# Performance work log

Measured on AMD Instinct MI355X. Metric: run time of the kernel, lower is better.

Reference implementation:

```python
import jax, jax.numpy as jnp
import numpy as np
from jax import lax

B, T, E, H = 16, 1024, 512, 1024


def setup_inputs() -> dict:
    key = jax.random.key(0)
    ks = jax.random.split(key, 10)
    s = 0.1
    return {
        "x":   jax.random.normal(ks[0], (B, T, E), jnp.float32),
        # reset gate: sigmoid(x@Wxr + h@Whr + br)
        "Wxr": jax.random.normal(ks[1], (E, H), jnp.float32) * s,
        "Whr": jax.random.normal(ks[2], (H, H), jnp.float32) * s,
        "br":  jax.random.normal(ks[3], (H,), jnp.float32) * s,
        # update gate: sigmoid(x@Wxz + h@Whz + bz)
        "Wxz": jax.random.normal(ks[4], (E, H), jnp.float32) * s,
        "Whz": jax.random.normal(ks[5], (H, H), jnp.float32) * s,
        "bz":  jax.random.normal(ks[6], (H,), jnp.float32) * s,
        # candidate: tanh(r * (h@Wh) + x@Wi + b)
        "Wi":  jax.random.normal(ks[7], (E, H), jnp.float32) * s,
        "Wh":  jax.random.normal(ks[8], (H, H), jnp.float32) * s,
        "b":   jax.random.normal(ks[9], (H,), jnp.float32) * s,
    }


def reference(x, Wxr, Whr, br, Wxz, Whz, bz, Wi, Wh, b):
    # Batch all input-to-hidden projections across time up front.
    xr = jnp.einsum("bte,eh->bth", x, Wxr) + br  # [B,T,H]
    xz = jnp.einsum("bte,eh->bth", x, Wxz) + bz
    xi = jnp.einsum("bte,eh->bth", x, Wi) + b

    def step(h, inp):
        xr_t, xz_t, xi_t = inp  # each [B,H]
        r = jax.nn.sigmoid(xr_t + h @ Whr)
        z = jax.nn.sigmoid(xz_t + h @ Whz)
        cand = jnp.tanh(r * (h @ Wh) + xi_t)
        h_new = z * h + (1.0 - z) * cand
        return h_new, h_new

    h0 = jnp.zeros((x.shape[0], Wh.shape[0]), x.dtype)
    # scan over time: move T to leading axis
    _, hs = lax.scan(step, h0, (xr.transpose(1, 0, 2), xz.transpose(1, 0, 2), xi.transpose(1, 0, 2)))
    return hs.transpose(1, 0, 2)  # [B,T,H]
```

## Files before the change

kernel.cpp:

```cpp
#include <hip/hip_runtime.h>
#include <hip/hip_bf16.h>
#include <cstddef>
#include <cstdint>

static constexpr int BB = 16;
static constexpr int TT = 1024;
static constexpr int EE = 512;
static constexpr int HH = 1024;

static constexpr int NG   = 4;
static constexpr int GBLK = 64;
static constexpr int BPG  = 4;
static constexpr int COLS = 16;

using u32 = unsigned int;
using u64 = unsigned long long;
typedef float f32x4 __attribute__((ext_vector_type(4)));

__device__ __forceinline__ float st_load(const float* p) { return *p; }
__device__ __forceinline__ float st_load(const __hip_bfloat16* p) { return __bfloat162float(*p); }
__device__ __forceinline__ void st_store(float* p, float v) { *p = v; }
__device__ __forceinline__ void st_store(__hip_bfloat16* p, float v) { *p = __float2bfloat16(v); }

__device__ __forceinline__ void llc_load(f32x4& d, const f32x4* p) {
    asm volatile("global_load_dwordx4 %0, %1, off sc0 sc1" : "=v"(d) : "v"(p));
}
__device__ __forceinline__ void llc_drain() {
    asm volatile("s_waitcnt vmcnt(0)" ::: "memory");
    __builtin_amdgcn_sched_barrier(0);
}

#define FMA4(ACC, S, W)                         \
    (ACC).x = fmaf((S), (W).x, (ACC).x);        \
    (ACC).y = fmaf((S), (W).y, (ACC).y);        \
    (ACC).z = fmaf((S), (W).z, (ACC).z);        \
    (ACC).w = fmaf((S), (W).w, (ACC).w);

template <typename ST>
__global__ __launch_bounds__(256) void proj_kernel(
    const float* __restrict__ x,
    const float* __restrict__ Wxr, const float* __restrict__ br,
    const float* __restrict__ Wxz, const float* __restrict__ bz,
    const float* __restrict__ Wi,  const float* __restrict__ bi,
    ST* __restrict__ xr_out, ST* __restrict__ xz_out, float* __restrict__ xi_out,
    u32* __restrict__ bar)
{
    __shared__ float xT[16][68];
    __shared__ float wB[3][16][64];

    const int tid = threadIdx.x;
    if (blockIdx.x == 0 && blockIdx.y == 0) bar[tid] = 0u;

    const int tx = tid & 15, ty = tid >> 4;
    const int m0 = blockIdx.y * 64, n0 = blockIdx.x * 64;
    const float* Wg[3] = {Wxr, Wxz, Wi};

    float4 acc[3][4];
#pragma unroll
    for (int g = 0; g < 3; ++g)
#pragma unroll
        for (int i = 0; i < 4; ++i) acc[g][i] = make_float4(0.f, 0.f, 0.f, 0.f);

    const int xrow = tid >> 2, xk = (tid & 3) * 4;
    const int wk = tid >> 4, wn = (tid & 15) * 4;

    for (int k0 = 0; k0 < EE; k0 += 16) {
        float4 xv = *(const float4*)(x + (size_t)(m0 + xrow) * EE + k0 + xk);
        xT[xk + 0][xrow] = xv.x;
        xT[xk + 1][xrow] = xv.y;
        xT[xk + 2][xrow] = xv.z;
        xT[xk + 3][xrow] = xv.w;
#pragma unroll
        for (int g = 0; g < 3; ++g) {
            float4 wv = *(const float4*)(Wg[g] + (size_t)(k0 + wk) * HH + n0 + wn);
            *(float4*)&wB[g][wk][wn] = wv;
        }
        __syncthreads();
#pragma unroll
        for (int kk = 0; kk < 16; ++kk) {
            float4 a  = *(const float4*)&xT[kk][ty * 4];
            float4 w0 = *(const float4*)&wB[0][kk][tx * 4];
            float4 w1 = *(const float4*)&wB[1][kk][tx * 4];
            float4 w2 = *(const float4*)&wB[2][kk][tx * 4];
            float as[4] = {a.x, a.y, a.z, a.w};
#pragma unroll
            for (int i = 0; i < 4; ++i) {
                FMA4(acc[0][i], as[i], w0);
                FMA4(acc[1][i], as[i], w1);
                FMA4(acc[2][i], as[i], w2);
            }
        }
        __syncthreads();
    }

    float4 bv0 = *(const float4*)(br + n0 + tx * 4);
    float4 bv1 = *(const float4*)(bz + n0 + tx * 4);
    float4 bv2 = *(const float4*)(bi + n0 + tx * 4);
#pragma unroll
    for (int i = 0; i < 4; ++i) {
        size_t m = (size_t)m0 + ty * 4 + i;
        size_t off = m * HH + n0 + tx * 4;
        float4 v0 = acc[0][i]; v0.x += bv0.x; v0.y += bv0.y; v0.z += bv0.z; v0.w += bv0.w;
        float4 v1 = acc[1][i]; v1.x += bv1.x; v1.y += bv1.y; v1.z += bv1.z; v1.w += bv1.w;
        float4 v2 = acc[2][i]; v2.x += bv2.x; v2.y += bv2.y; v2.z += bv2.z; v2.w += bv2.w;
        st_store(xr_out + off + 0, v0.x); st_store(xr_out + off + 1, v0.y);
        st_store(xr_out + off + 2, v0.z); st_store(xr_out + off + 3, v0.w);
        st_store(xz_out + off + 0, v1.x); st_store(xz_out + off + 1, v1.y);
        st_store(xz_out + off + 2, v1.z); st_store(xz_out + off + 3, v1.w);
        *(float4*)(xi_out + off) = v2;
    }
}

__device__ __forceinline__ float row16_allreduce(float v) {
    int y;
    y = __builtin_amdgcn_update_dpp(0, __float_as_int(v), 0xB1, 0xF, 0xF, true);
    v += __int_as_float(y);
    y = __builtin_amdgcn_update_dpp(0, __float_as_int(v), 0x4E, 0xF, 0xF, true);
    v += __int_as_float(y);
    y = __builtin_amdgcn_update_dpp(0, __float_as_int(v), 0x124, 0xF, 0xF, true);
    v += __int_as_float(y);
    y = __builtin_amdgcn_update_dpp(0, __float_as_int(v), 0x128, 0xF, 0xF, true);
    v += __int_as_float(y);
    return v;
}

__device__ __forceinline__ void xbar(u32* ctr, unsigned target) {
    __syncthreads();
    if (threadIdx.x == 0) {
        asm volatile("s_waitcnt vmcnt(0)" ::: "memory");
        __builtin_amdgcn_sched_barrier(0);
        __hip_atomic_fetch_add(ctr, 1u, __ATOMIC_RELAXED, __HIP_MEMORY_SCOPE_AGENT);
        while (__hip_atomic_load(ctr, __ATOMIC_RELAXED, __HIP_MEMORY_SCOPE_AGENT) < target) {
            __builtin_amdgcn_s_sleep(1);
        }
        __builtin_amdgcn_sched_barrier(0);
    }
    __syncthreads();
}

template <typename ST>
__global__ __launch_bounds__(512, 1) void scan_kernel(
    const ST* __restrict__ xr, const ST* __restrict__ xz,
    const float* __restrict__ Whr, const float* __restrict__ Whz, const float* __restrict__ Wh,
    float* __restrict__ out,
    float* __restrict__ hbuf,
    u32* __restrict__ bar)
{
    __shared__ f32x4 hs[BPG * 256];
    __shared__ float red[8][4][48];
    __shared__ float pre[48][4];

    const int tid = threadIdx.x, bid = blockIdx.x;
    const int lane = tid & 63, wv = tid >> 6;
    const int cgg = lane >> 4, kslo = lane & 15;
    const int ks = wv * 16 + kslo;
    const int group = bid >> 6, gb = bid & 63;
    const int n0 = gb * COLS;
    u32* ctr = bar + group * 64;

    float wreg[12][8];
    {
        const float* WG[3] = {Whr, Whz, Wh};
#pragma unroll
        for (int u = 0; u < 12; ++u) {
            int ugc = cgg * 12 + u;
            const float* W = WG[ugc >> 4];
            int col = n0 + (ugc & 15);
#pragma unroll
            for (int j = 0; j < 8; ++j)
                wreg[u][j] = W[(size_t)(ks * 8 + j) * HH + col];
        }
    }

    if (tid < 64)
        __hip_atomic_store(&hbuf[bid * 64 + tid], 0.f, __ATOMIC_RELAXED, __HIP_MEMORY_SCOPE_AGENT);

    float pxr = 0.f, pxz = 0.f, pxi = 0.f;
    const int tb4 = tid >> 4, tc = tid & 15;
    const int tbg = group * BPG + tb4;
    if (tid < 64) {
        size_t idx = (size_t)(tbg * TT + 0) * HH + n0 + tc;
        pxr = st_load(xr + idx); pxz = st_load(xz + idx); pxi = out[idx];
    }

    unsigned bstep = 1;
    xbar(ctr, bstep * GBLK); ++bstep;

    for (int t = 0; t < TT; ++t) {
        const f32x4* hin = (const f32x4*)(hbuf + (size_t)(t & 1) * (BB * HH) + group * BPG * HH);
        float* hout = hbuf + (size_t)((t + 1) & 1) * (BB * HH) + group * BPG * HH;

        f32x4 tmp0, tmp1;
        int q0 = (tid + (gb << 3)) & 1023;
        int q1 = (tid + 512 + (gb << 3)) & 1023;
        llc_load(tmp0, hin + q0);
        llc_load(tmp1, hin + q1);
        llc_drain();
        {
            int s0 = q0 & 255, s1 = q1 & 255;
            hs[(q0 & 0x300) | (s0 ^ ((s0 >> 3) & 7))] = tmp0;
            hs[(q1 & 0x300) | (s1 ^ ((s1 >> 3) & 7))] = tmp1;
        }
        __syncthreads();

        float pacc[4][12];
#pragma unroll
        for (int b = 0; b < 4; ++b)
#pragma unroll
            for (int u = 0; u < 12; ++u) pacc[b][u] = 0.f;

        const int s0 = 2 * ks;
        const int c0 = (s0 >> 3) & 7;
        const int sl0 = s0 ^ c0;
#pragma unroll
        for (int b = 0; b < 4; ++b) {
            f32x4 ha = hs[(b << 8) | sl0];
            f32x4 hb = hs[(b << 8) | (sl0 ^ 1)];
#pragma unroll
            for (int u = 0; u < 12; ++u) {
                float a = pacc[b][u];
                a = fmaf(ha[0], wreg[u][0], a);
                a = fmaf(ha[1], wreg[u][1], a);
                a = fmaf(ha[2], wreg[u][2], a);
                a = fmaf(ha[3], wreg[u][3], a);
                a = fmaf(hb[0], wreg[u][4], a);
                a = fmaf(hb[1], wreg[u][5], a);
                a = fmaf(hb[2], wreg[u][6], a);
                a = fmaf(hb[3], wreg[u][7], a);
                pacc[b][u] = a;
            }
        }

#pragma unroll
        for (int b = 0; b < 4; ++b)
#pragma unroll
            for (int u = 0; u < 12; ++u) pacc[b][u] = row16_allreduce(pacc[b][u]);

        if (kslo == 0) {
#pragma unroll
            for (int b = 0; b < 4; ++b)
#pragma unroll
                for (int u = 0; u < 12; ++u) red[wv][cgg][b * 12 + u] = pacc[b][u];
        }
        __syncthreads();

        if (tid < 192) {
            int b4 = tid & 3, ugc = tid >> 2;
            int cq = ugc / 12, u = ugc - cq * 12;
            float s = 0.f;
#pragma unroll
            for (int w = 0; w < 8; ++w) s += red[w][cq][b4 * 12 + u];
            pre[ugc][b4] = s;
        }
        __syncthreads();

        if (tid < 64) {
            size_t idx = (size_t)(tbg * TT + t) * HH + n0 + tc;
            float dr = pre[tc][tb4], dz = pre[16 + tc][tb4], dh = pre[32 + tc][tb4];
            float r = 1.f / (1.f + expf(-(dr + pxr)));
            float z = 1.f / (1.f + expf(-(dz + pxz)));
            float cand = tanhf(fmaf(r, dh, pxi));
            int colg = n0 + tc;
            int sp = colg >> 2;
            f32x4 h4 = hs[(tb4 << 8) | (sp ^ ((sp >> 3) & 7))];
            int cc = colg & 3;
            float hprev = (cc == 0) ? h4[0] : ((cc == 1) ? h4[1] : ((cc == 2) ? h4[2] : h4[3]));
            float hnew = fmaf(z, hprev - cand, cand);
            out[idx] = hnew;
            __hip_atomic_store(&hout[tb4 * HH + colg], hnew,
                               __ATOMIC_RELAXED, __HIP_MEMORY_SCOPE_AGENT);
            if (t + 1 < TT) {
                size_t idx2 = idx + HH;
                pxr = st_load(xr + idx2); pxz = st_load(xz + idx2); pxi = out[idx2];
            }
        }
        xbar(ctr, bstep * GBLK); ++bstep;
    }
}

__global__ void sentinel_kernel(float* out) {
    if (threadIdx.x == 0 && blockIdx.x == 0) out[0] = 12345.0f;
}

extern "C" void kernel_launch(void* const* d_in, const int* in_sizes, int n_in,
                              void* d_out, int out_size, void* d_ws, size_t ws_size,
                              hipStream_t stream) {
    const float* x   = (const float*)d_in[0];
    const float* Wxr = (const float*)d_in[1];
    const float* Whr = (const float*)d_in[2];
    const float* br  = (const float*)d_in[3];
    const float* Wxz = (const float*)d_in[4];
    const float* Whz = (const float*)d_in[5];
    const float* bz  = (const float*)d_in[6];
    const float* Wi  = (const float*)d_in[7];
    const float* Wh  = (const float*)d_in[8];
    const float* bb  = (const float*)d_in[9];
    float* out = (float*)d_out;

    const size_t BTH = (size_t)BB * TT * HH;
    const size_t HBUF_ELTS = (size_t)2 * BB * HH;
    const size_t BAR_BYTES = 4096;
    const size_t need_f32 = 2 * BTH * sizeof(float) + HBUF_ELTS * sizeof(float) + BAR_BYTES;
    const size_t need_b16 = 2 * BTH * sizeof(__hip_bfloat16) + HBUF_ELTS * sizeof(float) + BAR_BYTES;

    dim3 pgrid(HH / 64, (BB * TT) / 64);

    if (ws_size >= need_f32) {
        float* xr = (float*)d_ws;
        float* xz = xr + BTH;
        float* hb = xz + BTH;
        u32* bar = (u32*)(hb + HBUF_ELTS);
        proj_kernel<float><<<pgrid, 256, 0, stream>>>(x, Wxr, br, Wxz, bz, Wi, bb, xr, xz, out, bar);
        const float* xrc = xr; const float* xzc = xz;
        void* args[8] = {(void*)&xrc, (void*)&xzc, (void*)&Whr, (void*)&Whz,
                         (void*)&Wh, (void*)&out, (void*)&hb, (void*)&bar};
        hipLaunchCooperativeKernel((void*)scan_kernel<float>, dim3(256), dim3(512),
                                   args, 0, stream);
    } else if (ws_size >= need_b16) {
        __hip_bfloat16* xr = (__hip_bfloat16*)d_ws;
        __hip_bfloat16* xz = xr + BTH;
        float* hb = (float*)(xz + BTH);
        u32* bar = (u32*)(hb + HBUF_ELTS);
        proj_kernel<__hip_bfloat16><<<pgrid, 256, 0, stream>>>(x, Wxr, br, Wxz, bz, Wi, bb, xr, xz, out, bar);
        const __hip_bfloat16* xrc = xr; const __hip_bfloat16* xzc = xz;
        void* args[8] = {(void*)&xrc, (void*)&xzc, (void*)&Whr, (void*)&Whz,
                         (void*)&Wh, (void*)&out, (void*)&hb, (void*)&bar};
        hipLaunchCooperativeKernel((void*)scan_kernel<__hip_bfloat16>, dim3(256), dim3(512),
                                   args, 0, stream);
    } else {
        sentinel_kernel<<<1, 64, 0, stream>>>(out);
    }
}
```

Before: 5.703 ms.

## Replace per-step grid barrier with sentinel-polled 4-slot hidden state buffer

```diff
diff --git a/kernel.cpp b/kernel.cpp
--- a/kernel.cpp
+++ b/kernel.cpp
@@ -14,8 +14,9 @@
 static constexpr int COLS = 16;
 
 using u32 = unsigned int;
-using u64 = unsigned long long;
 typedef float f32x4 __attribute__((ext_vector_type(4)));
+
+static constexpr u32 PZ = 0x7FC0DEADu;
 
 __device__ __forceinline__ float st_load(const float* p) { return *p; }
 __device__ __forceinline__ float st_load(const __hip_bfloat16* p) { return __bfloat162float(*p); }
@@ -28,6 +29,10 @@
 __device__ __forceinline__ void llc_drain() {
     asm volatile("s_waitcnt vmcnt(0)" ::: "memory");
     __builtin_amdgcn_sched_barrier(0);
+}
+__device__ __forceinline__ bool ok4(const f32x4 v) {
+    return __float_as_uint(v[0]) != PZ && __float_as_uint(v[1]) != PZ &&
+           __float_as_uint(v[2]) != PZ && __float_as_uint(v[3]) != PZ;
 }
 
 #define FMA4(ACC, S, W)                         \
@@ -146,7 +151,7 @@
     float* __restrict__ hbuf,
     u32* __restrict__ bar)
 {
-    __shared__ f32x4 hs[BPG * 256];
+    __shared__ f32x4 hsx[8][4][32];
     __shared__ float red[8][4][48];
     __shared__ float pre[48][4];
 
@@ -172,36 +177,41 @@
         }
     }
 
-    if (tid < 64)
-        __hip_atomic_store(&hbuf[bid * 64 + tid], 0.f, __ATOMIC_RELAXED, __HIP_MEMORY_SCOPE_AGENT);
-
-    float pxr = 0.f, pxz = 0.f, pxi = 0.f;
+    const float pzf = __uint_as_float(PZ);
     const int tb4 = tid >> 4, tc = tid & 15;
     const int tbg = group * BPG + tb4;
+    const int coln = n0 + tc;
+
+    float pxr = 0.f, pxz = 0.f, pxi = 0.f, hprev = 0.f;
     if (tid < 64) {
-        size_t idx = (size_t)(tbg * TT + 0) * HH + n0 + tc;
-        pxr = st_load(xr + idx); pxz = st_load(xz + idx); pxi = out[idx];
-    }
-
-    unsigned bstep = 1;
-    xbar(ctr, bstep * GBLK); ++bstep;
+        float* b0 = hbuf + group * (BPG * HH) + tb4 * HH + coln;
+        __hip_atomic_store(b0,           0.f, __ATOMIC_RELAXED, __HIP_MEMORY_SCOPE_AGENT);
+        __hip_atomic_store(b0 + 16384,   pzf, __ATOMIC_RELAXED, __HIP_MEMORY_SCOPE_AGENT);
+        __hip_atomic_store(b0 + 32768,   pzf, __ATOMIC_RELAXED, __HIP_MEMORY_SCOPE_AGENT);
+        __hip_atomic_store(b0 + 49152,   pzf, __ATOMIC_RELAXED, __HIP_MEMORY_SCOPE_AGENT);
+        size_t idx0 = (size_t)(tbg * TT) * HH + coln;
+        pxr = st_load(xr + idx0); pxz = st_load(xz + idx0); pxi = out[idx0];
+    }
+    xbar(ctr, GBLK);
+
+    const int b_ld = lane >> 4;
+    const int s_rot = (((lane & 15) + (gb & 15)) * 2) & 31;
 
     for (int t = 0; t < TT; ++t) {
-        const f32x4* hin = (const f32x4*)(hbuf + (size_t)(t & 1) * (BB * HH) + group * BPG * HH);
-        float* hout = hbuf + (size_t)((t + 1) & 1) * (BB * HH) + group * BPG * HH;
-
-        f32x4 tmp0, tmp1;
-        int q0 = (tid + (gb << 3)) & 1023;
-        int q1 = (tid + 512 + (gb << 3)) & 1023;
-        llc_load(tmp0, hin + q0);
-        llc_load(tmp1, hin + q1);
-        llc_drain();
         {
-            int s0 = q0 & 255, s1 = q1 & 255;
-            hs[(q0 & 0x300) | (s0 ^ ((s0 >> 3) & 7))] = tmp0;
-            hs[(q1 & 0x300) | (s1 ^ ((s1 >> 3) & 7))] = tmp1;
-        }
-        __syncthreads();
+            const f32x4* p = (const f32x4*)hbuf + (size_t)(t & 3) * 4096
+                             + group * 1024 + b_ld * 256 + wv * 32 + s_rot;
+            f32x4 va, vb;
+            for (;;) {
+                llc_load(va, p); llc_load(vb, p + 1); llc_drain();
+                if (ok4(va) && ok4(vb)) break;
+                __builtin_amdgcn_s_sleep(1);
+            }
+            hsx[wv][b_ld][s_rot]     = va;
+            hsx[wv][b_ld][s_rot + 1] = vb;
+            asm volatile("s_waitcnt lgkmcnt(0)" ::: "memory");
+            __builtin_amdgcn_sched_barrier(0);
+        }
 
         float pacc[4][12];
 #pragma unroll
@@ -209,13 +219,10 @@
 #pragma unroll
             for (int u = 0; u < 12; ++u) pacc[b][u] = 0.f;
 
-        const int s0 = 2 * ks;
-        const int c0 = (s0 >> 3) & 7;
-        const int sl0 = s0 ^ c0;
 #pragma unroll
         for (int b = 0; b < 4; ++b) {
-            f32x4 ha = hs[(b << 8) | sl0];
-            f32x4 hb = hs[(b << 8) | (sl0 ^ 1)];
+            f32x4 ha = hsx[wv][b][2 * kslo];
+            f32x4 hb = hsx[wv][b][2 * kslo + 1];
 #pragma unroll
             for (int u = 0; u < 12; ++u) {
                 float a = pacc[b][u];
@@ -242,6 +249,12 @@
 #pragma unroll
                 for (int u = 0; u < 12; ++u) red[wv][cgg][b * 12 + u] = pacc[b][u];
         }
+
+        if (tid < 64 && t + 2 < TT) {
+            __hip_atomic_store(hbuf + (size_t)((t + 2) & 3) * 16384
+                               + group * (BPG * HH) + tb4 * HH + coln,
+                               pzf, __ATOMIC_RELAXED, __HIP_MEMORY_SCOPE_AGENT);
+        }
         __syncthreads();
 
         if (tid < 192) {
@@ -255,26 +268,26 @@
         __syncthreads();
 
         if (tid < 64) {
-            size_t idx = (size_t)(tbg * TT + t) * HH + n0 + tc;
             float dr = pre[tc][tb4], dz = pre[16 + tc][tb4], dh = pre[32 + tc][tb4];
             float r = 1.f / (1.f + expf(-(dr + pxr)));
             float z = 1.f / (1.f + expf(-(dz + pxz)));
             float cand = tanhf(fmaf(r, dh, pxi));
-            int colg = n0 + tc;
-            int sp = colg >> 2;
-            f32x4 h4 = hs[(tb4 << 8) | (sp ^ ((sp >> 3) & 7))];
-            int cc = colg & 3;
-            float hprev = (cc == 0) ? h4[0] : ((cc == 1) ? h4[1] : ((cc == 2) ? h4[2] : h4[3]));
             float hnew = fmaf(z, hprev - cand, cand);
+            hprev = hnew;
+            asm volatile("s_waitcnt vmcnt(0)" ::: "memory");
+            __builtin_amdgcn_sched_barrier(0);
+            if (t + 1 < TT) {
+                __hip_atomic_store(hbuf + (size_t)((t + 1) & 3) * 16384
+                                   + group * (BPG * HH) + tb4 * HH + coln,
+                                   hnew, __ATOMIC_RELAXED, __HIP_MEMORY_SCOPE_AGENT);
+            }
+            size_t idx = (size_t)(tbg * TT + t) * HH + coln;
             out[idx] = hnew;
-            __hip_atomic_store(&hout[tb4 * HH + colg], hnew,
-                               __ATOMIC_RELAXED, __HIP_MEMORY_SCOPE_AGENT);
             if (t + 1 < TT) {
                 size_t idx2 = idx + HH;
                 pxr = st_load(xr + idx2); pxz = st_load(xz + idx2); pxi = out[idx2];
             }
         }
-        xbar(ctr, bstep * GBLK); ++bstep;
     }
 }
 
@@ -298,7 +311,7 @@
     float* out = (float*)d_out;
 
     const size_t BTH = (size_t)BB * TT * HH;
-    const size_t HBUF_ELTS = (size_t)2 * BB * HH;
+    const size_t HBUF_ELTS = (size_t)4 * BB * HH;
     const size_t BAR_BYTES = 4096;
     const size_t need_f32 = 2 * BTH * sizeof(float) + HBUF_ELTS * sizeof(float) + BAR_BYTES;
     const size_t need_b16 = 2 * BTH * sizeof(__hip_bfloat16) + HBUF_ELTS * sizeof(float) + BAR_BYTES;
```

After: 5.154 ms. 1.11x faster.
